# Optimization experiments

Hardware: AMD Instinct MI355X
Metric: run time of the kernel (lower is better)

## Reference

```python
import jax, jax.numpy as jnp
import numpy as np

D, H, COND, MLP_RATIO = 1024, 16, 1024, 4
HD = D // H
DFF = MLP_RATIO * D


def layer_norm(x, w, eps=1e-5):
    xf = x.astype(jnp.float32)
    mu = jnp.mean(xf, axis=-1, keepdims=True)
    var = jnp.mean((xf - mu) ** 2, axis=-1, keepdims=True)
    return (xf - mu) * jax.lax.rsqrt(var + eps) * w


def rms_norm(x, w, eps=1e-6):
    xf = x.astype(jnp.float32)
    rms = jnp.sqrt(jnp.mean(xf * xf, axis=-1, keepdims=True) + eps)
    return (xf / rms * w).astype(x.dtype)


def rotate_half(x):
    x1, x2 = x[..., : x.shape[-1] // 2], x[..., x.shape[-1] // 2:]
    return jnp.concatenate([-x2, x1], axis=-1)


def apply_rope(x, cos, sin):
    return x * cos + rotate_half(x) * sin


def setup_inputs() -> dict:
    key = jax.random.key(0)
    ks = jax.random.split(key, 16)
    B, S = 4, 2048
    pos = jnp.arange(S, dtype=jnp.float32)
    inv = 1.0 / (10000.0 ** (jnp.arange(0, HD, 2, dtype=jnp.float32) / HD))
    freqs = pos[:, None] * inv[None, :]              # (S, HD/2)
    emb = jnp.concatenate([freqs, freqs], axis=-1)   # (S, HD)
    return {
        "x": jax.random.normal(ks[0], (B, S, D), jnp.float32),
        "cos": jnp.cos(emb)[None, :, None, :],        # (1,S,1,HD)
        "sin": jnp.sin(emb)[None, :, None, :],
        "c": jax.random.normal(ks[1], (B, COND), jnp.float32),
        "norm1_w": jnp.ones((D,), jnp.float32),
        "Wqkv": jax.random.normal(ks[2], (D, 3 * D), jnp.float32) * 0.02,
        "Wout": jax.random.normal(ks[3], (D, D), jnp.float32) * 0.02,
        "q_norm_w": jnp.ones((HD,), jnp.float32),
        "k_norm_w": jnp.ones((HD,), jnp.float32),
        "norm2_w": jnp.ones((D,), jnp.float32),
        "W1": jax.random.normal(ks[4], (D, DFF), jnp.float32) * 0.02,
        "b1": jnp.zeros((DFF,), jnp.float32),
        "W2": jax.random.normal(ks[5], (DFF, D), jnp.float32) * 0.02,
        "b2": jnp.zeros((D,), jnp.float32),
        "ada_W": jax.random.normal(ks[6], (COND, 6 * D), jnp.float32) * 0.02,
        "ada_b": jnp.zeros((6 * D,), jnp.float32),
    }


def reference(x, cos, sin, c, norm1_w, Wqkv, Wout, q_norm_w, k_norm_w,
              norm2_w, W1, b1, W2, b2, ada_W, ada_b):
    B, S, _ = x.shape
    mod = (c @ ada_W + ada_b)[:, None, :]            # (B,1,6D)
    sh_msa, sc_msa, g_msa, sh_mlp, sc_mlp, g_mlp = jnp.split(mod, 6, axis=-1)

    x_norm = layer_norm(x, norm1_w) * (1 + sc_msa) + sh_msa
    qkv = (x_norm @ Wqkv).reshape(B, S, 3, H, HD)
    q, k, v = qkv[:, :, 0], qkv[:, :, 1], qkv[:, :, 2]  # (B,S,H,HD)
    q = apply_rope(rms_norm(q, q_norm_w), cos, sin)
    k = apply_rope(rms_norm(k, k_norm_w), cos, sin)

    scale = 1.0 / jnp.sqrt(jnp.float32(HD))
    logits = jnp.einsum('bqhd,bkhd->bhqk', q, k) * scale
    probs = jax.nn.softmax(logits, axis=-1)
    attn = jnp.einsum('bhqk,bkhd->bqhd', probs, v).reshape(B, S, D)

    x = x + g_msa * (attn @ Wout)

    x_norm = layer_norm(x, norm2_w) * (1 + sc_mlp) + sh_mlp
    h = jax.nn.gelu(x_norm @ W1 + b1, approximate=True)
    x = x + g_mlp * (h @ W2 + b2)
    return x
```

## Files before the change

kernel.cpp:

```cpp
#include <hip/hip_runtime.h>
#include <hip/hip_bf16.h>
#include <math.h>

typedef __bf16 bf16;
typedef __bf16 bf16x8 __attribute__((ext_vector_type(8)));
typedef __bf16 bf16x4 __attribute__((ext_vector_type(4)));
typedef float f32x4 __attribute__((ext_vector_type(4)));
typedef short s16x4 __attribute__((ext_vector_type(4)));

#define S_LEN 2048
#define NTOK 8192
#define DIM 1024
#define NH 16
#define HEADD 64
#define DFF 4096
#define MODD 6144

__device__ __forceinline__ float gelu_tanh(float x) {
  float inner = 0.7978845608028654f * (x + 0.044715f * x * x * x);
  return 0.5f * x * (1.0f + tanhf(inner));
}

__global__ __launch_bounds__(256) void init_mod_kernel(
    const float* __restrict__ ada_b, float* __restrict__ mod) {
  int i = blockIdx.x * 256 + threadIdx.x;
  mod[i] = ada_b[i % MODD];
}

__global__ __launch_bounds__(256) void ada_gemm_kernel(
    const float* __restrict__ cnd, const float* __restrict__ W,
    float* __restrict__ mod) {
  int n = blockIdx.x * 256 + threadIdx.x;
  int k0 = blockIdx.y * 128;
  float a0 = 0.f, a1 = 0.f, a2 = 0.f, a3 = 0.f;
  for (int k = k0; k < k0 + 128; ++k) {
    float w = W[(size_t)k * MODD + n];
    a0 = fmaf(cnd[k], w, a0);
    a1 = fmaf(cnd[1024 + k], w, a1);
    a2 = fmaf(cnd[2048 + k], w, a2);
    a3 = fmaf(cnd[3072 + k], w, a3);
  }
  atomicAdd(&mod[n], a0);
  atomicAdd(&mod[MODD + n], a1);
  atomicAdd(&mod[2 * MODD + n], a2);
  atomicAdd(&mod[3 * MODD + n], a3);
}

__global__ __launch_bounds__(256) void transpose_cast_kernel(
    const float* __restrict__ W, bf16* __restrict__ Wt, int K, int N) {
  __shared__ float tile[32][33];
  int n0 = blockIdx.x * 32, k0 = blockIdx.y * 32;
  int r = threadIdx.x >> 3;
  int c4 = (threadIdx.x & 7) * 4;
  float4 v = *(const float4*)&W[(size_t)(k0 + r) * N + n0 + c4];
  tile[r][c4 + 0] = v.x; tile[r][c4 + 1] = v.y;
  tile[r][c4 + 2] = v.z; tile[r][c4 + 3] = v.w;
  __syncthreads();
  bf16x4 o;
  o[0] = (bf16)tile[c4 + 0][r];
  o[1] = (bf16)tile[c4 + 1][r];
  o[2] = (bf16)tile[c4 + 2][r];
  o[3] = (bf16)tile[c4 + 3][r];
  *(bf16x4*)&Wt[(size_t)(n0 + r) * K + k0 + c4] = o;
}

__global__ __launch_bounds__(256) void vtrans_kernel(
    const bf16* __restrict__ qkv, bf16* __restrict__ VT) {
  __shared__ __align__(16) bf16 t[64][72];
  const int bh = blockIdx.y;
  const int b = bh >> 4, h = bh & 15;
  const int s0 = blockIdx.x * 64;
  const int tid = threadIdx.x;
  {
    const int r = tid >> 2;
    const int c = (tid & 3) * 16;
    const bf16* src =
        qkv + (size_t)(b * S_LEN + s0 + r) * 3072 + 2048 + h * 64 + c;
    *(bf16x8*)&t[r][c] = *(const bf16x8*)src;
    *(bf16x8*)&t[r][c + 8] = *(const bf16x8*)(src + 8);
  }
  __syncthreads();
  {
    const int d = tid & 63;
    const int sc = (tid >> 6) * 16;
    bf16x8 o0, o1;
#pragma unroll
    for (int j = 0; j < 8; ++j) o0[j] = t[sc + j][d];
#pragma unroll
    for (int j = 0; j < 8; ++j) o1[j] = t[sc + 8 + j][d];
    bf16* dst = VT + (size_t)(bh * 64 + d) * S_LEN + s0 + sc;
    *(bf16x8*)dst = o0;
    *(bf16x8*)(dst + 8) = o1;
  }
}

__global__ __launch_bounds__(256) void ln_mod_kernel(
    const float* __restrict__ x, const float* __restrict__ w,
    const float* __restrict__ mod, int sh_off, int sc_off,
    bf16* __restrict__ out) {
  __shared__ float red[8];
  const int row = blockIdx.x;
  const int b = row >> 11;
  const int tid = threadIdx.x;
  const float4 v = ((const float4*)(x + (size_t)row * DIM))[tid];
  float s1 = v.x + v.y + v.z + v.w;
  float s2 = v.x * v.x + v.y * v.y + v.z * v.z + v.w * v.w;
  for (int off = 32; off > 0; off >>= 1) {
    s1 += __shfl_down(s1, off, 64);
    s2 += __shfl_down(s2, off, 64);
  }
  const int wid = tid >> 6;
  if ((tid & 63) == 0) { red[wid] = s1; red[4 + wid] = s2; }
  __syncthreads();
  s1 = red[0] + red[1] + red[2] + red[3];
  s2 = red[4] + red[5] + red[6] + red[7];
  const float mu = s1 * (1.0f / DIM);
  const float inv = rsqrtf(s2 * (1.0f / DIM) - mu * mu + 1e-5f);
  const int c = tid * 4;
  const float* mb = mod + (size_t)b * MODD;
  float xs[4] = {v.x, v.y, v.z, v.w};
  bf16x4 o;
#pragma unroll
  for (int j = 0; j < 4; ++j)
    o[j] = (bf16)(((xs[j] - mu) * inv) * w[c + j] * (1.0f + mb[sc_off + c + j]) +
                  mb[sh_off + c + j]);
  *(bf16x4*)(out + (size_t)row * DIM + c) = o;
}

template <int EPI, int MT, int BN>
__global__ __launch_bounds__(256) void gemm_bt(
    const bf16* __restrict__ A, const bf16* __restrict__ Bt,
    bf16* __restrict__ Cb, float* __restrict__ Cf,
    const float* __restrict__ bias, const float* __restrict__ gmod,
    const float* __restrict__ resid, const float* __restrict__ cosb,
    const float* __restrict__ sinb, const float* __restrict__ qw,
    const float* __restrict__ kw, int M, int N, int K) {
  constexpr int IM = MT / 32;
  constexpr int JN = BN / 32;
  constexpr int NA = MT / 64;
  constexpr int NB = BN / 64;
  __shared__ __align__(16) bf16 As[2][MT * 32];
  __shared__ __align__(16) bf16 Bs[2][BN * 32];
  const int tid = threadIdx.x;
  const int wid = tid >> 6;
  const int lane = tid & 63;
  const int l15 = lane & 15;
  const int quad = lane >> 4;
  const int m0 = blockIdx.y * MT;
  const int n0 = blockIdx.x * BN;
  const int wm = (wid & 1) * (MT / 2);
  const int wn = (wid >> 1) * (BN / 2);

  const int r0 = tid >> 2;
  const int cc0 = (tid & 3) * 8;
  const bf16* Ap = A + (size_t)(m0 + r0) * K + cc0;
  const bf16* Bp = Bt + (size_t)(n0 + r0) * K + cc0;

  bf16x8 ar[NA][2], br[NB][2];
#pragma unroll
  for (int g = 0; g < NA; ++g)
#pragma unroll
    for (int hf = 0; hf < 2; ++hf)
      ar[g][hf] = *(const bf16x8*)(Ap + (size_t)g * 64 * K + hf * 32);
#pragma unroll
  for (int g = 0; g < NB; ++g)
#pragma unroll
    for (int hf = 0; hf < 2; ++hf)
      br[g][hf] = *(const bf16x8*)(Bp + (size_t)g * 64 * K + hf * 32);

  f32x4 acc[IM][JN] = {};

  for (int kt = 0; kt < K; kt += 64) {
    __syncthreads();
#pragma unroll
    for (int g = 0; g < NA; ++g)
#pragma unroll
      for (int hf = 0; hf < 2; ++hf)
        *(bf16x8*)&As[hf][(g * 256 + tid) * 8] = ar[g][hf];
#pragma unroll
    for (int g = 0; g < NB; ++g)
#pragma unroll
      for (int hf = 0; hf < 2; ++hf)
        *(bf16x8*)&Bs[hf][(g * 256 + tid) * 8] = br[g][hf];
    __syncthreads();
    if (kt + 64 < K) {
#pragma unroll
      for (int g = 0; g < NA; ++g)
#pragma unroll
        for (int hf = 0; hf < 2; ++hf)
          ar[g][hf] = *(const bf16x8*)(Ap + (size_t)g * 64 * K + kt + 64 + hf * 32);
#pragma unroll
      for (int g = 0; g < NB; ++g)
#pragma unroll
        for (int hf = 0; hf < 2; ++hf)
          br[g][hf] = *(const bf16x8*)(Bp + (size_t)g * 64 * K + kt + 64 + hf * 32);
    }
#pragma unroll
    for (int half = 0; half < 2; ++half) {
      bf16x8 af[IM], bfr[JN];
#pragma unroll
      for (int i = 0; i < IM; ++i)
        af[i] = *(const bf16x8*)&As[half][(wm + i * 16 + l15) * 32 + quad * 8];
#pragma unroll
      for (int j = 0; j < JN; ++j)
        bfr[j] = *(const bf16x8*)&Bs[half][(wn + j * 16 + l15) * 32 + quad * 8];
#pragma unroll
      for (int i = 0; i < IM; ++i)
#pragma unroll
        for (int j = 0; j < JN; ++j)
          acc[i][j] = __builtin_amdgcn_mfma_f32_16x16x32_bf16(af[i], bfr[j],
                                                              acc[i][j], 0, 0, 0);
    }
  }

  if (EPI == 4 && n0 < 2048) {
    const float* nw = ((n0 + wn) < 1024) ? qw : kw;
    float wv[4];
#pragma unroll
    for (int j = 0; j < 4; ++j) wv[j] = nw[j * 16 + l15];
#pragma unroll
    for (int i = 0; i < IM; ++i) {
#pragma unroll
      for (int r = 0; r < 4; ++r) {
        const int m = m0 + wm + i * 16 + quad * 4 + r;
        const int s = m & (S_LEN - 1);
        float v[4];
        float ss = 0.f;
#pragma unroll
        for (int j = 0; j < 4; ++j) { v[j] = acc[i][j][r]; ss += v[j] * v[j]; }
        ss += __shfl_xor(ss, 1, 64);
        ss += __shfl_xor(ss, 2, 64);
        ss += __shfl_xor(ss, 4, 64);
        ss += __shfl_xor(ss, 8, 64);
        const float inv = rsqrtf(ss * (1.0f / HEADD) + 1e-6f);
        float xn[4];
#pragma unroll
        for (int j = 0; j < 4; ++j) xn[j] = v[j] * inv * wv[j];
#pragma unroll
        for (int j = 0; j < 4; ++j) {
          const int d = j * 16 + l15;
          const float rot = (j < 2) ? -xn[j + 2] : xn[j - 2];
          const float o = xn[j] * cosb[s * HEADD + d] + rot * sinb[s * HEADD + d];
          Cb[(size_t)m * N + n0 + wn + d] = (bf16)o;
        }
      }
    }
    return;
  }

#pragma unroll
  for (int i = 0; i < IM; ++i) {
#pragma unroll
    for (int r = 0; r < 4; ++r) {
      const int m = m0 + wm + i * 16 + quad * 4 + r;
#pragma unroll
      for (int j = 0; j < JN; ++j) {
        const int n = n0 + wn + j * 16 + l15;
        float v = acc[i][j][r];
        if (EPI == 0 || EPI == 4) {
          Cb[(size_t)m * N + n] = (bf16)v;
        } else if (EPI == 1) {
          const int b = m >> 11;
          Cf[(size_t)m * N + n] =
              resid[(size_t)m * N + n] + gmod[(size_t)b * MODD + n] * v;
        } else if (EPI == 2) {
          v += bias[n];
          Cb[(size_t)m * N + n] = (bf16)gelu_tanh(v);
        } else {
          v += bias[n];
          const int b = m >> 11;
          Cf[(size_t)m * N + n] =
              resid[(size_t)m * N + n] + gmod[(size_t)b * MODD + n] * v;
        }
      }
    }
  }
}

__global__ __launch_bounds__(256) void attn_kernel(
    const bf16* __restrict__ qkv, const bf16* __restrict__ VT,
    bf16* __restrict__ Opart, float* __restrict__ psumbuf) {
  __shared__ __align__(16) bf16 Ks[4096];
  __shared__ __align__(16) bf16 Vs[4096];
  const int bh = blockIdx.y;
  const int b = bh >> 4;
  const int h = bh & 15;
  const int q0 = blockIdx.x * 128;
  const int split = blockIdx.z;
  const int tid = threadIdx.x;
  const int wid = tid >> 6;
  const int lane = tid & 63;
  const int l15 = lane & 15;
  const int quad = lane >> 4;

  bf16x8 aq[2][2];
#pragma unroll
  for (int i = 0; i < 2; ++i) {
    const int qrow = q0 + wid * 32 + i * 16 + l15;
    const size_t qbase = (size_t)(b * S_LEN + qrow) * (3 * DIM) + h * HEADD;
    aq[i][0] = *(const bf16x8*)(qkv + qbase + quad * 8);
    aq[i][1] = *(const bf16x8*)(qkv + qbase + 32 + quad * 8);
  }

  const int rstage = lane;
  const int rsw = rstage & 7;
  const bf16* krow =
      qkv + (size_t)(b * S_LEN + split * 1024 + rstage) * 3072 + DIM + h * HEADD;
  const bf16* vrow = VT + (size_t)(bh * 64 + rstage) * S_LEN + split * 1024;

  bf16x8 kreg[2], vreg[2];
#pragma unroll
  for (int rr = 0; rr < 2; ++rr) {
    const int ck = wid + 4 * rr;
    kreg[rr] = *(const bf16x8*)(krow + ck * 8);
    vreg[rr] = *(const bf16x8*)(vrow + ck * 8);
  }

  const float cexp = 0.125f * 1.44269504f;
  f32x4 oacc[2][4] = {};
  float psum[2] = {0.f, 0.f};

  for (int t = 0; t < 16; ++t) {
    __syncthreads();
#pragma unroll
    for (int rr = 0; rr < 2; ++rr) {
      const int ck = wid + 4 * rr;
      const int sw = ((ck ^ rsw) << 3);
      *(bf16x8*)&Ks[rstage * 64 + sw] = kreg[rr];
      *(bf16x8*)&Vs[rstage * 64 + sw] = vreg[rr];
    }
    __syncthreads();
    if (t < 15) {
      krow += 64 * 3072;
      vrow += 64;
#pragma unroll
      for (int rr = 0; rr < 2; ++rr) {
        const int ck = wid + 4 * rr;
        kreg[rr] = *(const bf16x8*)(krow + ck * 8);
        vreg[rr] = *(const bf16x8*)(vrow + ck * 8);
      }
    }

    f32x4 sc[2][4] = {};
#pragma unroll
    for (int hh = 0; hh < 2; ++hh) {
#pragma unroll
      for (int cc = 0; cc < 4; ++cc) {
        const int row = cc * 16 + l15;
        const bf16x8 kf =
            *(const bf16x8*)&Ks[row * 64 + (((quad + 4 * hh) ^ (l15 & 7)) << 3)];
#pragma unroll
        for (int i = 0; i < 2; ++i)
          sc[i][cc] = __builtin_amdgcn_mfma_f32_16x16x32_bf16(kf, aq[i][hh],
                                                              sc[i][cc], 0, 0, 0);
      }
    }

    s16x4 pf[2][4];
#pragma unroll
    for (int i = 0; i < 2; ++i)
#pragma unroll
      for (int cc = 0; cc < 4; ++cc) {
        bf16x4 pb;
#pragma unroll
        for (int r = 0; r < 4; ++r) {
          const float p = __builtin_amdgcn_exp2f(fmaf(sc[i][cc][r], cexp, -8.0f));
          psum[i] += p;
          pb[r] = (bf16)p;
        }
        pf[i][cc] = __builtin_bit_cast(s16x4, pb);
      }

#pragma unroll
    for (int j = 0; j < 4; ++j) {
      const int d = 16 * j + l15;
      const int drow = d * 64;
      const int dsw = d & 7;
#pragma unroll
      for (int cc = 0; cc < 4; ++cc) {
        const int ck = 2 * cc + (quad >> 1);
        const s16x4 vf =
            *(const s16x4*)&Vs[drow + ((ck ^ dsw) << 3) + ((quad & 1) << 2)];
#pragma unroll
        for (int i = 0; i < 2; ++i)
          oacc[i][j] = __builtin_amdgcn_mfma_f32_16x16x16bf16_1k(pf[i][cc], vf,
                                                                 oacc[i][j], 0, 0, 0);
      }
    }
  }

#pragma unroll
  for (int i = 0; i < 2; ++i) {
    float ps = psum[i];
    ps += __shfl_xor(ps, 16, 64);
    ps += __shfl_xor(ps, 32, 64);
    if (lane < 16) {
      const int qrow = q0 + wid * 32 + i * 16 + lane;
      psumbuf[(size_t)split * (NTOK * NH) + (size_t)(b * S_LEN + qrow) * NH + h] = ps;
    }
#pragma unroll
    for (int r = 0; r < 4; ++r) {
      const int m = q0 + wid * 32 + i * 16 + quad * 4 + r;
#pragma unroll
      for (int j = 0; j < 4; ++j)
        Opart[(size_t)split * (NTOK * DIM) +
              ((size_t)(b * S_LEN + m) * NH + h) * HEADD + j * 16 + l15] =
            (bf16)oacc[i][j][r];
    }
  }
}

__global__ __launch_bounds__(256) void attn_reduce_kernel(
    const bf16* __restrict__ Opart, const float* __restrict__ psumbuf,
    bf16* __restrict__ attn) {
  const int g = blockIdx.x * 256 + threadIdx.x;
  const int token = g >> 7;
  const int rem = g & 127;
  const int h = rem >> 3;
  const int d0 = (rem & 7) * 8;
  const size_t off = ((size_t)token * NH + h) * HEADD + d0;
  const bf16x8 o0 = *(const bf16x8*)(Opart + off);
  const bf16x8 o1 = *(const bf16x8*)(Opart + (size_t)NTOK * DIM + off);
  const float l = psumbuf[token * NH + h] + psumbuf[NTOK * NH + token * NH + h];
  const float invl = 1.0f / l;
  bf16x8 o;
#pragma unroll
  for (int j = 0; j < 8; ++j)
    o[j] = (bf16)(((float)o0[j] + (float)o1[j]) * invl);
  *(bf16x8*)(attn + off) = o;
}

extern "C" void kernel_launch(void* const* d_in, const int* in_sizes, int n_in,
                              void* d_out, int out_size, void* d_ws,
                              size_t ws_size, hipStream_t stream) {
  const float* x = (const float*)d_in[0];
  const float* cosb = (const float*)d_in[1];
  const float* sinb = (const float*)d_in[2];
  const float* cnd = (const float*)d_in[3];
  const float* norm1_w = (const float*)d_in[4];
  const float* Wqkv = (const float*)d_in[5];
  const float* Wout = (const float*)d_in[6];
  const float* q_norm_w = (const float*)d_in[7];
  const float* k_norm_w = (const float*)d_in[8];
  const float* norm2_w = (const float*)d_in[9];
  const float* W1 = (const float*)d_in[10];
  const float* b1 = (const float*)d_in[11];
  const float* W2 = (const float*)d_in[12];
  const float* b2 = (const float*)d_in[13];
  const float* ada_W = (const float*)d_in[14];
  const float* ada_b = (const float*)d_in[15];
  float* out = (float*)d_out;

  char* p = (char*)d_ws;
  float* mod = (float*)p;   p += (size_t)4 * MODD * 4;
  bf16* WqkvT = (bf16*)p;   p += (size_t)3072 * 1024 * 2;
  bf16* WoutT = (bf16*)p;   p += (size_t)1024 * 1024 * 2;
  bf16* W1T = (bf16*)p;     p += (size_t)4096 * 1024 * 2;
  bf16* W2T = (bf16*)p;     p += (size_t)1024 * 4096 * 2;
  bf16* XN = (bf16*)p;      p += (size_t)NTOK * DIM * 2;
  bf16* QKV = (bf16*)p;     p += (size_t)NTOK * 3 * DIM * 2;
  bf16* ATTN = (bf16*)p;    p += (size_t)NTOK * DIM * 2;
  bf16* Hbuf = (bf16*)p;    p += (size_t)NTOK * DFF * 2;
  bf16* VT = Hbuf;
  bf16* Opart = Hbuf + (size_t)NTOK * DIM;
  float* psumbuf = (float*)(Hbuf + (size_t)3 * NTOK * DIM);

  init_mod_kernel<<<96, 256, 0, stream>>>(ada_b, mod);
  ada_gemm_kernel<<<dim3(24, 8), 256, 0, stream>>>(cnd, ada_W, mod);
  transpose_cast_kernel<<<dim3(96, 32), 256, 0, stream>>>(Wqkv, WqkvT, 1024, 3072);
  transpose_cast_kernel<<<dim3(32, 32), 256, 0, stream>>>(Wout, WoutT, 1024, 1024);
  transpose_cast_kernel<<<dim3(128, 32), 256, 0, stream>>>(W1, W1T, 1024, 4096);
  transpose_cast_kernel<<<dim3(32, 128), 256, 0, stream>>>(W2, W2T, 4096, 1024);
  ln_mod_kernel<<<NTOK, 256, 0, stream>>>(x, norm1_w, mod, 0, 1024, XN);
  gemm_bt<4, 128, 128><<<dim3(24, 64), 256, 0, stream>>>(
      XN, WqkvT, QKV, nullptr, nullptr, nullptr, nullptr, cosb, sinb,
      q_norm_w, k_norm_w, NTOK, 3072, 1024);
  vtrans_kernel<<<dim3(32, 64), 256, 0, stream>>>(QKV, VT);
  attn_kernel<<<dim3(16, 64, 2), 256, 0, stream>>>(QKV, VT, Opart, psumbuf);
  attn_reduce_kernel<<<4096, 256, 0, stream>>>(Opart, psumbuf, ATTN);
  gemm_bt<1, 128, 64><<<dim3(16, 64), 256, 0, stream>>>(
      ATTN, WoutT, nullptr, out, nullptr, mod + 2 * 1024, x, nullptr, nullptr,
      nullptr, nullptr, NTOK, 1024, 1024);
  ln_mod_kernel<<<NTOK, 256, 0, stream>>>(out, norm2_w, mod, 3 * 1024, 4 * 1024, XN);
  gemm_bt<2, 128, 128><<<dim3(32, 64), 256, 0, stream>>>(
      XN, W1T, Hbuf, nullptr, b1, nullptr, nullptr, nullptr, nullptr,
      nullptr, nullptr, NTOK, DFF, 1024);
  gemm_bt<3, 128, 64><<<dim3(16, 64), 256, 0, stream>>>(
      Hbuf, W2T, nullptr, out, b2, mod + 5 * 1024, out, nullptr, nullptr,
      nullptr, nullptr, NTOK, 1024, DFF);
  (void)in_sizes; (void)n_in; (void)out_size; (void)ws_size;
}
```

Before: 634.3 us.

## Load GEMM tiles directly to LDS via global_load_lds and enlarge N tiles

Replaces the register-staged prefetch of A/B tiles in the bf16 GEMM with direct global-to-LDS loads (global_load_lds, 16 bytes per lane), shrinking the K step from 64 to 32 and dropping the register double buffer. This frees VGPRs and removes the register-to-LDS store instructions. The catch is that the next tile's load is no longer overlapped with compute, since loads and MFMA are separated by barriers each step. The Wout and W2 GEMMs also move from 128x64 to 128x128 tiles, halving their grids.

```diff
diff --git a/kernel.cpp b/kernel.cpp
--- a/kernel.cpp
+++ b/kernel.cpp
@@ -19,6 +19,12 @@
 __device__ __forceinline__ float gelu_tanh(float x) {
   float inner = 0.7978845608028654f * (x + 0.044715f * x * x * x);
   return 0.5f * x * (1.0f + tanhf(inner));
+}
+
+__device__ __forceinline__ void gl_lds16(const bf16* g, bf16* l) {
+  __builtin_amdgcn_global_load_lds(
+      (const __attribute__((address_space(1))) unsigned int*)g,
+      (__attribute__((address_space(3))) unsigned int*)l, 16, 0, 0);
 }
 
 __global__ __launch_bounds__(256) void init_mod_kernel(
@@ -137,10 +143,10 @@
     const float* __restrict__ kw, int M, int N, int K) {
   constexpr int IM = MT / 32;
   constexpr int JN = BN / 32;
-  constexpr int NA = MT / 64;
-  constexpr int NB = BN / 64;
-  __shared__ __align__(16) bf16 As[2][MT * 32];
-  __shared__ __align__(16) bf16 Bs[2][BN * 32];
+  constexpr int AG = MT / 64;
+  constexpr int BG = BN / 64;
+  __shared__ __align__(16) bf16 As[MT * 32];
+  __shared__ __align__(16) bf16 Bs[BN * 32];
   const int tid = threadIdx.x;
   const int wid = tid >> 6;
   const int lane = tid & 63;
@@ -151,66 +157,36 @@
   const int wm = (wid & 1) * (MT / 2);
   const int wn = (wid >> 1) * (BN / 2);
 
-  const int r0 = tid >> 2;
-  const int cc0 = (tid & 3) * 8;
-  const bf16* Ap = A + (size_t)(m0 + r0) * K + cc0;
-  const bf16* Bp = Bt + (size_t)(n0 + r0) * K + cc0;
-
-  bf16x8 ar[NA][2], br[NB][2];
-#pragma unroll
-  for (int g = 0; g < NA; ++g)
-#pragma unroll
-    for (int hf = 0; hf < 2; ++hf)
-      ar[g][hf] = *(const bf16x8*)(Ap + (size_t)g * 64 * K + hf * 32);
-#pragma unroll
-  for (int g = 0; g < NB; ++g)
-#pragma unroll
-    for (int hf = 0; hf < 2; ++hf)
-      br[g][hf] = *(const bf16x8*)(Bp + (size_t)g * 64 * K + hf * 32);
+  const int srow = wid * 16 + (lane >> 2);
+  const int scol = (lane & 3) * 8;
+  const bf16* Ap = A + (size_t)(m0 + srow) * K + scol;
+  const bf16* Bp = Bt + (size_t)(n0 + srow) * K + scol;
 
   f32x4 acc[IM][JN] = {};
 
-  for (int kt = 0; kt < K; kt += 64) {
+  for (int kt = 0; kt < K; kt += 32) {
     __syncthreads();
 #pragma unroll
-    for (int g = 0; g < NA; ++g)
-#pragma unroll
-      for (int hf = 0; hf < 2; ++hf)
-        *(bf16x8*)&As[hf][(g * 256 + tid) * 8] = ar[g][hf];
-#pragma unroll
-    for (int g = 0; g < NB; ++g)
-#pragma unroll
-      for (int hf = 0; hf < 2; ++hf)
-        *(bf16x8*)&Bs[hf][(g * 256 + tid) * 8] = br[g][hf];
+    for (int g = 0; g < AG; ++g)
+      gl_lds16(Ap + (size_t)g * 64 * K + kt, As + g * 2048 + wid * 512);
+#pragma unroll
+    for (int g = 0; g < BG; ++g)
+      gl_lds16(Bp + (size_t)g * 64 * K + kt, Bs + g * 2048 + wid * 512);
     __syncthreads();
-    if (kt + 64 < K) {
-#pragma unroll
-      for (int g = 0; g < NA; ++g)
-#pragma unroll
-        for (int hf = 0; hf < 2; ++hf)
-          ar[g][hf] = *(const bf16x8*)(Ap + (size_t)g * 64 * K + kt + 64 + hf * 32);
-#pragma unroll
-      for (int g = 0; g < NB; ++g)
-#pragma unroll
-        for (int hf = 0; hf < 2; ++hf)
-          br[g][hf] = *(const bf16x8*)(Bp + (size_t)g * 64 * K + kt + 64 + hf * 32);
-    }
-#pragma unroll
-    for (int half = 0; half < 2; ++half) {
-      bf16x8 af[IM], bfr[JN];
-#pragma unroll
-      for (int i = 0; i < IM; ++i)
-        af[i] = *(const bf16x8*)&As[half][(wm + i * 16 + l15) * 32 + quad * 8];
+
+    bf16x8 af[IM], bfr[JN];
+#pragma unroll
+    for (int i = 0; i < IM; ++i)
+      af[i] = *(const bf16x8*)&As[(wm + i * 16 + l15) * 32 + quad * 8];
+#pragma unroll
+    for (int j = 0; j < JN; ++j)
+      bfr[j] = *(const bf16x8*)&Bs[(wn + j * 16 + l15) * 32 + quad * 8];
+#pragma unroll
+    for (int i = 0; i < IM; ++i)
 #pragma unroll
       for (int j = 0; j < JN; ++j)
-        bfr[j] = *(const bf16x8*)&Bs[half][(wn + j * 16 + l15) * 32 + quad * 8];
-#pragma unroll
-      for (int i = 0; i < IM; ++i)
-#pragma unroll
-        for (int j = 0; j < JN; ++j)
-          acc[i][j] = __builtin_amdgcn_mfma_f32_16x16x32_bf16(af[i], bfr[j],
-                                                              acc[i][j], 0, 0, 0);
-    }
+        acc[i][j] = __builtin_amdgcn_mfma_f32_16x16x32_bf16(af[i], bfr[j],
+                                                            acc[i][j], 0, 0, 0);
   }
 
   if (EPI == 4 && n0 < 2048) {
@@ -478,14 +454,14 @@
   vtrans_kernel<<<dim3(32, 64), 256, 0, stream>>>(QKV, VT);
   attn_kernel<<<dim3(16, 64, 2), 256, 0, stream>>>(QKV, VT, Opart, psumbuf);
   attn_reduce_kernel<<<4096, 256, 0, stream>>>(Opart, psumbuf, ATTN);
-  gemm_bt<1, 128, 64><<<dim3(16, 64), 256, 0, stream>>>(
+  gemm_bt<1, 128, 128><<<dim3(8, 64), 256, 0, stream>>>(
       ATTN, WoutT, nullptr, out, nullptr, mod + 2 * 1024, x, nullptr, nullptr,
       nullptr, nullptr, NTOK, 1024, 1024);
   ln_mod_kernel<<<NTOK, 256, 0, stream>>>(out, norm2_w, mod, 3 * 1024, 4 * 1024, XN);
   gemm_bt<2, 128, 128><<<dim3(32, 64), 256, 0, stream>>>(
       XN, W1T, Hbuf, nullptr, b1, nullptr, nullptr, nullptr, nullptr,
       nullptr, nullptr, NTOK, DFF, 1024);
-  gemm_bt<3, 128, 64><<<dim3(16, 64), 256, 0, stream>>>(
+  gemm_bt<3, 128, 128><<<dim3(8, 64), 256, 0, stream>>>(
       Hbuf, W2T, nullptr, out, b2, mod + 5 * 1024, out, nullptr, nullptr,
       nullptr, nullptr, NTOK, 1024, DFF);
   (void)in_sizes; (void)n_in; (void)out_size; (void)ws_size;
```

After: 670.7 us. +5.7%, slower.
